# Kernel optimization log

Measured on AMD Instinct MI355X. Metric: run time of the kernel, lower is better.

Reference implementation:

```python
import jax, jax.numpy as jnp
import numpy as np

DIM = 1024
HEADS = 16
DIM_HEAD = DIM // HEADS
SCALE = DIM_HEAD ** -0.5


def setup_inputs() -> dict:
    key = jax.random.key(0)
    k1, k2, k3 = jax.random.split(key, 3)
    x = jax.random.normal(k1, (4, 2048, DIM), dtype=jnp.float32)
    # q_lin: Linear(dim, 3*dim, bias=False); store as [dim, 3*dim] for x @ W
    w_qkv = jax.random.normal(k2, (DIM, 3 * DIM), dtype=jnp.float32) * (DIM ** -0.5)
    w_out = jax.random.normal(k3, (DIM, DIM), dtype=jnp.float32) * (DIM ** -0.5)
    return {"x": x, "w_qkv": w_qkv, "w_out": w_out}


def reference(x, w_qkv, w_out):
    b, n, d = x.shape
    qkv = x @ w_qkv  # [b, n, 3d]
    q, k, v = jnp.split(qkv, 3, axis=-1)
    # b n (h d) -> b h n d
    def to_heads(t):
        return t.reshape(b, n, HEADS, DIM_HEAD).transpose(0, 2, 1, 3)
    q, k, v = to_heads(q), to_heads(k), to_heads(v)
    sim = jnp.einsum('bhnj,bhmj->bhnm', q, k) * SCALE
    causal = jnp.triu(jnp.ones((n, n), dtype=bool), k=1)
    sim = jnp.where(causal, -jnp.finfo(sim.dtype).max, sim)
    attn = jax.nn.softmax(sim, axis=-1)
    out = jnp.einsum('bhnm,bhmd->bhnd', attn, v)
    out = out.transpose(0, 2, 1, 3).reshape(b, n, d)  # b h n d -> b n (h d)
    return out @ w_out
```

## Files before the change

kernel.cpp:

```cpp
#include <hip/hip_runtime.h>
#include <hip/hip_bf16.h>
#include <stdint.h>

#define SEQ  2048
#define DIMM 1024
#define NH   16
#define DH   64
#define NB   4
#define MROWS (NB*SEQ)
#define QKP  2080

typedef __attribute__((ext_vector_type(8))) short bf16x8;
typedef __attribute__((ext_vector_type(4))) float f32x4;
typedef __attribute__((ext_vector_type(16))) float f32x16;

#define LOG2E 1.44269504088896340736f

__device__ __forceinline__ unsigned short f2bf(float f) {
    union { float f; uint32_t u; } c; c.f = f;
    uint32_t r = c.u + 0x7fff + ((c.u >> 16) & 1);
    return (unsigned short)(r >> 16);
}

__device__ __forceinline__ void gload_lds16(const void* g, void* lds) {
    __builtin_amdgcn_global_load_lds(
        (const __attribute__((address_space(1))) unsigned int*)(g),
        (__attribute__((address_space(3))) unsigned int*)(lds),
        16, 0, 0);
}

__global__ __launch_bounds__(256) void k_conv_bf16(const float* __restrict__ in,
                                                   unsigned short* __restrict__ out,
                                                   int n4) {
    int i = blockIdx.x * 256 + threadIdx.x;
    if (i >= n4) return;
    float4 v = ((const float4*)in)[i];
    ushort4 o;
    o.x = f2bf(v.x); o.y = f2bf(v.y); o.z = f2bf(v.z); o.w = f2bf(v.w);
    ((ushort4*)out)[i] = o;
}

__global__ __launch_bounds__(256) void k_transpose(const float* __restrict__ W,
                                                   unsigned short* __restrict__ Wt,
                                                   int K, int N) {
    __shared__ unsigned short tile[32][33];
    int tn = blockIdx.x, tk = blockIdx.y;
    int lx = threadIdx.x & 31, ly = threadIdx.x >> 5;
    #pragma unroll
    for (int i = 0; i < 32; i += 8) {
        int k = tk * 32 + ly + i;
        int n = tn * 32 + lx;
        tile[ly + i][lx] = f2bf(W[(size_t)k * N + n]);
    }
    __syncthreads();
    int k2 = tk * 32 + lx;
    #pragma unroll
    for (int i = 0; i < 32; i += 8) {
        int n2 = tn * 32 + ly + i;
        Wt[(size_t)n2 * K + k2] = tile[lx][ly + i];
    }
}

template<int MODE>
__global__ __launch_bounds__(256) void k_gemm_bt(const unsigned short* __restrict__ A,
                                                 const unsigned short* __restrict__ Bt,
                                                 void* __restrict__ Cv,
                                                 unsigned short* __restrict__ vtv,
                                                 int M, int N_, int K) {
    constexpr int BM = 128, BN = 128, BK = 64;
    __shared__ unsigned short lA[BM * BK];
    __shared__ unsigned short lB[BN * BK];
    const int ntile = N_ / BN;
    const int tm = blockIdx.x / ntile;
    const int tn = blockIdx.x % ntile;
    const int t = threadIdx.x;
    const int w = t >> 6, l = t & 63;
    const int wr = w >> 1, wc = w & 1;

    const unsigned short* Abase = A + (size_t)tm * BM * K;
    const unsigned short* Bbase = Bt + (size_t)tn * BN * K;

    f32x4 acc[4][4] = {};

    const int rswz = (l & 7) << 4;

    for (int k0 = 0; k0 < K; k0 += BK) {
        __syncthreads();
        #pragma unroll
        for (int i = 0; i < 4; ++i) {
            const int o  = i * 4096 + t * 16;
            const int so = o ^ (((o >> 7) & 7) << 4);
            const int row = so >> 7;
            const int kb  = so & 127;
            gload_lds16((const char*)(Abase + (size_t)row * K + k0) + kb,
                        (char*)lA + i * 4096 + w * 1024);
            gload_lds16((const char*)(Bbase + (size_t)row * K + k0) + kb,
                        (char*)lB + i * 4096 + w * 1024);
        }
        __syncthreads();

        #pragma unroll
        for (int kk = 0; kk < 2; ++kk) {
            bf16x8 af[4], bfv[4];
            #pragma unroll
            for (int i = 0; i < 4; ++i) {
                const int ea = ((wr * 64 + i * 16 + (l & 15)) << 7) + kk * 64 + ((l >> 4) << 4);
                af[i] = *(const bf16x8*)((const char*)lA + (ea ^ rswz));
            }
            #pragma unroll
            for (int j = 0; j < 4; ++j) {
                const int eb = ((wc * 64 + j * 16 + (l & 15)) << 7) + kk * 64 + ((l >> 4) << 4);
                bfv[j] = *(const bf16x8*)((const char*)lB + (eb ^ rswz));
            }
            #pragma unroll
            for (int i = 0; i < 4; ++i)
                #pragma unroll
                for (int j = 0; j < 4; ++j)
                    acc[i][j] = __builtin_amdgcn_mfma_f32_16x16x32_bf16(af[i], bfv[j], acc[i][j], 0, 0, 0);
        }
    }

    const int row0 = tm * BM + wr * 64 + (l >> 4) * 4;
    const int col0 = tn * BN + wc * 64 + (l & 15);

    if (MODE == 0) {
        float* Cf = (float*)Cv;
        #pragma unroll
        for (int i = 0; i < 4; ++i)
            #pragma unroll
            for (int j = 0; j < 4; ++j)
                #pragma unroll
                for (int r = 0; r < 4; ++r)
                    Cf[(size_t)(row0 + i * 16 + r) * N_ + (col0 + j * 16)] = acc[i][j][r];
    } else if (tn < 16) {
        const float cs = (tn < 8) ? 0.125f * LOG2E : 1.0f;
        unsigned short* qk = (unsigned short*)Cv;
        #pragma unroll
        for (int i = 0; i < 4; ++i)
            #pragma unroll
            for (int j = 0; j < 4; ++j)
                #pragma unroll
                for (int r = 0; r < 4; ++r)
                    qk[(size_t)(row0 + i * 16 + r) * QKP + (col0 + j * 16)] = f2bf(acc[i][j][r] * cs);
    } else {
        #pragma unroll
        for (int i = 0; i < 4; ++i) {
            const int rbase = row0 + i * 16;
            const int bq = rbase >> 11;
            const int n0 = rbase & 2047;
            #pragma unroll
            for (int j = 0; j < 4; ++j) {
                const int c = col0 + j * 16 - 2048;
                const int hh = c >> 6, dd = c & 63;
                uint2 u;
                u.x = (unsigned int)f2bf(acc[i][j][0]) | ((unsigned int)f2bf(acc[i][j][1]) << 16);
                u.y = (unsigned int)f2bf(acc[i][j][2]) | ((unsigned int)f2bf(acc[i][j][3]) << 16);
                *(uint2*)(vtv + ((size_t)(bq * 16 + hh) * 64 + dd) * QKP + n0) = u;
            }
        }
    }
}

__global__ __launch_bounds__(256, 2) void k_attn14(const unsigned short* __restrict__ qk,
                                                   const unsigned short* __restrict__ vt,
                                                   unsigned short* __restrict__ out) {
    const int wid = (blockIdx.x & 7) * 64 + (blockIdx.x >> 3);
    const int bh = wid >> 3;
    const int pair = wid & 7;
    const int b = bh >> 4, h = bh & 15;
    const int w = threadIdx.x >> 6, l = threadIdx.x & 63;
    const int l31 = l & 31, hi = l >> 5;

    const unsigned short* qp = qk + (size_t)(b * SEQ) * QKP + h * 64;
    unsigned short* op = out + (size_t)(b * SEQ) * DIMM + h * 64;

    constexpr int KSTEP = 64 * QKP * 2;
    constexpr int VSTEP = 64 * 2;

    union U8 { uint32_t u[4]; bf16x8 v; };

    for (int ci = 0; ci < 2; ++ci) {
        const int chunk = ci ? pair : 15 - pair;
        const int q0w = chunk * 128 + w * 32;
        const int qrow = q0w + l31;
        const int nt = (q0w >> 6) + 1;

        bf16x8 qf[4];
        #pragma unroll
        for (int m = 0; m < 4; ++m)
            qf[m] = *(const bf16x8*)(qp + (size_t)(q0w + l31) * QKP + m * 16 + hi * 8);

        f32x16 accO0 = {}, accO1 = {};
        float m_run = -INFINITY, l_run = 0.f;

        const char* kp0 = (const char*)(qk + ((size_t)b * SEQ + l31) * QKP + 1024 + h * 64 + hi * 8);
        const char* kp1 = kp0 + 32 * QKP * 2;
        const char* vp0 = (const char*)(vt + ((size_t)bh * 64 + l31) * QKP + hi * 8);
        const char* vp1 = vp0 + 32 * QKP * 2;

        bf16x8 kf[2][4];
        #pragma unroll
        for (int m = 0; m < 4; ++m) {
            kf[0][m] = *(const bf16x8*)(kp0 + m * 32);
            kf[1][m] = *(const bf16x8*)(kp1 + m * 32);
        }
        kp0 += KSTEP; kp1 += KSTEP;

        for (int kt = 0; kt < nt; ++kt) {
            const int kv0 = kt * 64;
            const bool msk = (kt == nt - 1);

            f32x16 s0 = {}, s1 = {};
            __builtin_amdgcn_s_setprio(1);
            #pragma unroll
            for (int m = 0; m < 4; ++m) {
                s0 = __builtin_amdgcn_mfma_f32_32x32x16_bf16(kf[0][m], qf[m], s0, 0, 0, 0);
                s1 = __builtin_amdgcn_mfma_f32_32x32x16_bf16(kf[1][m], qf[m], s1, 0, 0, 0);
            }
            __builtin_amdgcn_s_setprio(0);

            bf16x8 vf0[4], vf1[4];
            #pragma unroll
            for (int m = 0; m < 4; ++m) {
                vf0[m] = *(const bf16x8*)(vp0 + m * 32);
                vf1[m] = *(const bf16x8*)(vp1 + m * 32);
            }
            vp0 += VSTEP; vp1 += VSTEP;

            #pragma unroll
            for (int m = 0; m < 4; ++m) {
                kf[0][m] = *(const bf16x8*)(kp0 + m * 32);
                kf[1][m] = *(const bf16x8*)(kp1 + m * 32);
            }
            kp0 += KSTEP; kp1 += KSTEP;

            float tmax = -1e30f;
            #pragma unroll
            for (int r = 0; r < 16; ++r) {
                const int crow = (r & 3) + 8 * (r >> 2) + 4 * hi;
                float v0 = s0[r];
                float v1 = s1[r];
                if (msk) {
                    if (kv0 + crow > qrow)      v0 = -1e30f;
                    if (kv0 + 32 + crow > qrow) v1 = -1e30f;
                }
                s0[r] = v0; s1[r] = v1;
                tmax = fmaxf(tmax, fmaxf(v0, v1));
            }
            tmax = fmaxf(tmax, __shfl_xor(tmax, 32));
            const bool defer = __all(tmax <= m_run + 8.0f);
            float fct = 1.0f;
            if (!defer) {
                const float mnew = fmaxf(m_run, tmax);
                fct = exp2f(m_run - mnew);
                m_run = mnew;
                #pragma unroll
                for (int r = 0; r < 16; ++r) { accO0[r] *= fct; accO1[r] *= fct; }
            }
            float ps = 0.f;
            #pragma unroll
            for (int r = 0; r < 16; ++r) {
                float p0 = exp2f(s0[r] - m_run);
                float p1 = exp2f(s1[r] - m_run);
                s0[r] = p0; s1[r] = p1;
                ps += p0 + p1;
            }
            ps += __shfl_xor(ps, 32);
            l_run = l_run * fct + ps;

            uint32_t pw0[8], pw1[8];
            #pragma unroll
            for (int i = 0; i < 8; ++i) {
                asm("v_cvt_pk_bf16_f32 %0, %1, %2" : "=v"(pw0[i]) : "v"(s0[2*i]), "v"(s0[2*i+1]));
                asm("v_cvt_pk_bf16_f32 %0, %1, %2" : "=v"(pw1[i]) : "v"(s1[2*i]), "v"(s1[2*i+1]));
            }
            __builtin_amdgcn_s_setprio(1);
            #define PVCHUNK(PW, BASE, VF0, VF1) do {                                     \
                uint32_t a0 = PW[BASE+0], b0 = PW[BASE+2];                               \
                uint32_t a1 = PW[BASE+1], b1 = PW[BASE+3];                               \
                asm("v_permlane32_swap_b32 %0, %1" : "+v"(a0), "+v"(b0));                \
                asm("v_permlane32_swap_b32 %0, %1" : "+v"(a1), "+v"(b1));                \
                U8 pb; pb.u[0] = a0; pb.u[1] = a1; pb.u[2] = b0; pb.u[3] = b1;           \
                accO0 = __builtin_amdgcn_mfma_f32_32x32x16_bf16(VF0, pb.v, accO0, 0, 0, 0); \
                accO1 = __builtin_amdgcn_mfma_f32_32x32x16_bf16(VF1, pb.v, accO1, 0, 0, 0); \
            } while (0)
            PVCHUNK(pw0, 0, vf0[0], vf1[0]);
            PVCHUNK(pw0, 4, vf0[1], vf1[1]);
            PVCHUNK(pw1, 0, vf0[2], vf1[2]);
            PVCHUNK(pw1, 4, vf0[3], vf1[3]);
            #undef PVCHUNK
            __builtin_amdgcn_s_setprio(0);
        }

        const float inv = 1.0f / l_run;
        unsigned short* orow = op + (size_t)(q0w + l31) * DIMM;
        #pragma unroll
        for (int g = 0; g < 4; ++g) {
            uint2 u0, u1;
            float a0 = accO0[4*g+0] * inv, a1 = accO0[4*g+1] * inv;
            float a2 = accO0[4*g+2] * inv, a3 = accO0[4*g+3] * inv;
            float c0 = accO1[4*g+0] * inv, c1 = accO1[4*g+1] * inv;
            float c2 = accO1[4*g+2] * inv, c3 = accO1[4*g+3] * inv;
            asm("v_cvt_pk_bf16_f32 %0, %1, %2" : "=v"(u0.x) : "v"(a0), "v"(a1));
            asm("v_cvt_pk_bf16_f32 %0, %1, %2" : "=v"(u0.y) : "v"(a2), "v"(a3));
            asm("v_cvt_pk_bf16_f32 %0, %1, %2" : "=v"(u1.x) : "v"(c0), "v"(c1));
            asm("v_cvt_pk_bf16_f32 %0, %1, %2" : "=v"(u1.y) : "v"(c2), "v"(c3));
            *(uint2*)(orow + 8*g + 4*hi)      = u0;
            *(uint2*)(orow + 32 + 8*g + 4*hi) = u1;
        }
    }
}

extern "C" void kernel_launch(void* const* d_in, const int* in_sizes, int n_in,
                              void* d_out, int out_size, void* d_ws, size_t ws_size,
                              hipStream_t stream) {
    const float* x     = (const float*)d_in[0];
    const float* w_qkv = (const float*)d_in[1];
    const float* w_out = (const float*)d_in[2];

    unsigned short* x_bf   = (unsigned short*)d_ws;
    unsigned short* wqkvT  = x_bf   + (size_t)MROWS * DIMM;
    unsigned short* woutT  = wqkvT  + (size_t)3 * DIMM * DIMM;
    unsigned short* qk_buf = woutT  + (size_t)DIMM * DIMM;
    unsigned short* vt     = qk_buf + (size_t)MROWS * QKP;
    unsigned short* aout   = vt     + (size_t)64 * DH * QKP;

    k_conv_bf16<<<(MROWS * DIMM / 4 + 255) / 256, 256, 0, stream>>>(x, x_bf, MROWS * DIMM / 4);
    dim3 g1(3 * DIMM / 32, DIMM / 32);
    k_transpose<<<g1, 256, 0, stream>>>(w_qkv, wqkvT, DIMM, 3 * DIMM);
    dim3 g2(DIMM / 32, DIMM / 32);
    k_transpose<<<g2, 256, 0, stream>>>(w_out, woutT, DIMM, DIMM);

    k_gemm_bt<1><<<(MROWS / 128) * (3 * DIMM / 128), 256, 0, stream>>>(
        x_bf, wqkvT, qk_buf, vt, MROWS, 3 * DIMM, DIMM);

    k_attn14<<<NB * NH * 8, 256, 0, stream>>>(qk_buf, vt, aout);

    k_gemm_bt<0><<<(MROWS / 128) * (DIMM / 128), 256, 0, stream>>>(
        aout, woutT, d_out, nullptr, MROWS, DIMM, DIMM);
}
```

Before: 202.0 us.

## Merge prep kernels into one launch and shorten attention reduction chains

Folds the x-to-bf16 conversion and both weight transposes into a single prep kernel that dispatches on block index, cutting two kernel launches. In the attention kernel, the first MFMA of each score tile takes a zero accumulator directly instead of needing zero-initialized registers. The row max and row sum now use tree reductions over 16 values rather than serial chains, which shortens dependency latency at the cost of some extra live registers.

```diff
diff --git a/kernel.cpp b/kernel.cpp
--- a/kernel.cpp
+++ b/kernel.cpp
@@ -29,22 +29,33 @@
         16, 0, 0);
 }
 
-__global__ __launch_bounds__(256) void k_conv_bf16(const float* __restrict__ in,
-                                                   unsigned short* __restrict__ out,
-                                                   int n4) {
-    int i = blockIdx.x * 256 + threadIdx.x;
-    if (i >= n4) return;
-    float4 v = ((const float4*)in)[i];
-    ushort4 o;
-    o.x = f2bf(v.x); o.y = f2bf(v.y); o.z = f2bf(v.z); o.w = f2bf(v.w);
-    ((ushort4*)out)[i] = o;
-}
-
-__global__ __launch_bounds__(256) void k_transpose(const float* __restrict__ W,
-                                                   unsigned short* __restrict__ Wt,
-                                                   int K, int N) {
+__global__ __launch_bounds__(256) void k_prep(const float* __restrict__ x,
+                                              unsigned short* __restrict__ x_bf,
+                                              const float* __restrict__ w_qkv,
+                                              unsigned short* __restrict__ wqkvT,
+                                              const float* __restrict__ w_out,
+                                              unsigned short* __restrict__ woutT) {
     __shared__ unsigned short tile[32][33];
-    int tn = blockIdx.x, tk = blockIdx.y;
+    const int bid = blockIdx.x;
+    if (bid < 8192) {
+        int i = bid * 256 + threadIdx.x;
+        float4 v = ((const float4*)x)[i];
+        ushort4 o;
+        o.x = f2bf(v.x); o.y = f2bf(v.y); o.z = f2bf(v.z); o.w = f2bf(v.w);
+        ((ushort4*)x_bf)[i] = o;
+        return;
+    }
+    const float* W;
+    unsigned short* Wt;
+    int tn, tk, N;
+    if (bid < 8192 + 3072) {
+        W = w_qkv; Wt = wqkvT; N = 3072;
+        tn = (bid - 8192) % 96; tk = (bid - 8192) / 96;
+    } else {
+        W = w_out; Wt = woutT; N = 1024;
+        tn = (bid - 11264) % 32; tk = (bid - 11264) / 32;
+    }
+    const int K = 1024;
     int lx = threadIdx.x & 31, ly = threadIdx.x >> 5;
     #pragma unroll
     for (int i = 0; i < 32; i += 8) {
@@ -161,7 +172,7 @@
     }
 }
 
-__global__ __launch_bounds__(256, 2) void k_attn14(const unsigned short* __restrict__ qk,
+__global__ __launch_bounds__(256, 2) void k_attn15(const unsigned short* __restrict__ qk,
                                                    const unsigned short* __restrict__ vt,
                                                    unsigned short* __restrict__ out) {
     const int wid = (blockIdx.x & 7) * 64 + (blockIdx.x >> 3);
@@ -178,6 +189,7 @@
     constexpr int VSTEP = 64 * 2;
 
     union U8 { uint32_t u[4]; bf16x8 v; };
+    const f32x16 fz = {};
 
     for (int ci = 0; ci < 2; ++ci) {
         const int chunk = ci ? pair : 15 - pair;
@@ -210,12 +222,12 @@
             const int kv0 = kt * 64;
             const bool msk = (kt == nt - 1);
 
-            f32x16 s0 = {}, s1 = {};
+            f32x16 s0, s1;
             __builtin_amdgcn_s_setprio(1);
             #pragma unroll
             for (int m = 0; m < 4; ++m) {
-                s0 = __builtin_amdgcn_mfma_f32_32x32x16_bf16(kf[0][m], qf[m], s0, 0, 0, 0);
-                s1 = __builtin_amdgcn_mfma_f32_32x32x16_bf16(kf[1][m], qf[m], s1, 0, 0, 0);
+                s0 = __builtin_amdgcn_mfma_f32_32x32x16_bf16(kf[0][m], qf[m], m ? s0 : fz, 0, 0, 0);
+                s1 = __builtin_amdgcn_mfma_f32_32x32x16_bf16(kf[1][m], qf[m], m ? s1 : fz, 0, 0, 0);
             }
             __builtin_amdgcn_s_setprio(0);
 
@@ -234,7 +246,7 @@
             }
             kp0 += KSTEP; kp1 += KSTEP;
 
-            float tmax = -1e30f;
+            float mx[16];
             #pragma unroll
             for (int r = 0; r < 16; ++r) {
                 const int crow = (r & 3) + 8 * (r >> 2) + 4 * hi;
@@ -245,9 +257,13 @@
                     if (kv0 + 32 + crow > qrow) v1 = -1e30f;
                 }
                 s0[r] = v0; s1[r] = v1;
-                tmax = fmaxf(tmax, fmaxf(v0, v1));
-            }
-            tmax = fmaxf(tmax, __shfl_xor(tmax, 32));
+                mx[r] = fmaxf(v0, v1);
+            }
+            #pragma unroll
+            for (int d = 8; d; d >>= 1)
+                #pragma unroll
+                for (int r = 0; r < d; ++r) mx[r] = fmaxf(mx[r], mx[r + d]);
+            const float tmax = fmaxf(mx[0], __shfl_xor(mx[0], 32));
             const bool defer = __all(tmax <= m_run + 8.0f);
             float fct = 1.0f;
             if (!defer) {
@@ -257,16 +273,19 @@
                 #pragma unroll
                 for (int r = 0; r < 16; ++r) { accO0[r] *= fct; accO1[r] *= fct; }
             }
-            float ps = 0.f;
+            float pm[16];
             #pragma unroll
             for (int r = 0; r < 16; ++r) {
                 float p0 = exp2f(s0[r] - m_run);
                 float p1 = exp2f(s1[r] - m_run);
                 s0[r] = p0; s1[r] = p1;
-                ps += p0 + p1;
-            }
-            ps += __shfl_xor(ps, 32);
-            l_run = l_run * fct + ps;
+                pm[r] = p0 + p1;
+            }
+            #pragma unroll
+            for (int d = 8; d; d >>= 1)
+                #pragma unroll
+                for (int r = 0; r < d; ++r) pm[r] += pm[r + d];
+            l_run = l_run * fct + (pm[0] + __shfl_xor(pm[0], 32));
 
             uint32_t pw0[8], pw1[8];
             #pragma unroll
@@ -325,16 +344,12 @@
     unsigned short* vt     = qk_buf + (size_t)MROWS * QKP;
     unsigned short* aout   = vt     + (size_t)64 * DH * QKP;
 
-    k_conv_bf16<<<(MROWS * DIMM / 4 + 255) / 256, 256, 0, stream>>>(x, x_bf, MROWS * DIMM / 4);
-    dim3 g1(3 * DIMM / 32, DIMM / 32);
-    k_transpose<<<g1, 256, 0, stream>>>(w_qkv, wqkvT, DIMM, 3 * DIMM);
-    dim3 g2(DIMM / 32, DIMM / 32);
-    k_transpose<<<g2, 256, 0, stream>>>(w_out, woutT, DIMM, DIMM);
+    k_prep<<<8192 + 3072 + 1024, 256, 0, stream>>>(x, x_bf, w_qkv, wqkvT, w_out, woutT);
 
     k_gemm_bt<1><<<(MROWS / 128) * (3 * DIMM / 128), 256, 0, stream>>>(
         x_bf, wqkvT, qk_buf, vt, MROWS, 3 * DIMM, DIMM);
 
-    k_attn14<<<NB * NH * 8, 256, 0, stream>>>(qk_buf, vt, aout);
+    k_attn15<<<NB * NH * 8, 256, 0, stream>>>(qk_buf, vt, aout);
 
     k_gemm_bt<0><<<(MROWS / 128) * (DIMM / 128), 256, 0, stream>>>(
         aout, woutT, d_out, nullptr, MROWS, DIMM, DIMM);
```

Result: no change. 203.2 us (+0.6%).
